# Kernel tuning notes

Measured on AMD Instinct MI355X. Metric: run time of the kernel, lower is better.

Reference implementation:

```python
import jax, jax.numpy as jnp
import numpy as np

B, S, D, H, DO, E, K = 4, 2048, 1024, 4096, 1024, 8, 2


def setup_inputs() -> dict:
    key = jax.random.key(0)
    ks = jax.random.split(key, 5)
    sD = 1.0 / np.sqrt(D)
    sH = 1.0 / np.sqrt(H)
    return {
        "x": jax.random.normal(ks[0], (B, S, D), jnp.float32),
        "gate_w": jax.random.normal(ks[1], (D, E), jnp.float32) * sD,
        "gate_b": jnp.zeros((E,), jnp.float32),
        "w1": jax.random.normal(ks[2], (E, D, H), jnp.float32) * sD,
        "b1": jnp.zeros((E, H), jnp.float32),
        "w2": jax.random.normal(ks[3], (E, H, DO), jnp.float32) * sH,
        "b2": jnp.zeros((E, DO), jnp.float32),
    }


def reference(x, gate_w, gate_b, w1, b1, w2, b2):
    # Eval mode: no gating noise, dropout is identity.
    T = B * S
    xf = x.reshape(T, D)
    logits = xf @ gate_w + gate_b                      # [T, E]
    top_v, top_i = jax.lax.top_k(logits, K)            # [T, K]
    top_w = jax.nn.softmax(top_v, axis=-1)             # softmax over top-k scores
    # scatter top-k weights into dense [T, E] gate weights (indices are distinct)
    weights = jnp.zeros_like(logits).at[jnp.arange(T)[:, None], top_i].set(top_w)
    # dense per-expert MLP, combined with (mostly zero) gate weights —
    # same math as the masked gather/scatter loop in the torch source
    h = jax.nn.relu(jnp.einsum('td,edh->teh', xf, w1) + b1)   # [T, E, H]
    eo = jnp.einsum('teh,eho->teo', h, w2) + b2               # [T, E, DO]
    out = jnp.einsum('te,teo->to', weights, eo).reshape(B, S, DO)
    expert_usage = jnp.bincount(top_i.reshape(-1), length=E)
    return out, weights, expert_usage, top_i
```

## Files before the change

kernel.cpp:

```cpp
#include <hip/hip_runtime.h>
#include <cstdint>
#include <cstddef>

typedef unsigned short u16;
typedef unsigned int u32;
typedef short s16x8 __attribute__((ext_vector_type(8)));
typedef float f32x4 __attribute__((ext_vector_type(4)));

#define T_TOK 8192
#define D_IN  1024
#define H_DIM 4096
#define DO_DIM 1024

__device__ __forceinline__ u16 f2bf(float f) {
    u32 u = __float_as_uint(f);
    return (u16)((u + 0x7FFFu + ((u >> 16) & 1u)) >> 16);
}

__device__ __forceinline__ f32x4 mfma16(s16x8 a, s16x8 b, f32x4 c) {
    return __builtin_amdgcn_mfma_f32_16x16x32_bf16(a, b, c, 0, 0, 0);
}

__device__ __forceinline__ void gload16(const void* g, void* l) {
    __builtin_amdgcn_global_load_lds(
        (const __attribute__((address_space(1))) void*)g,
        (__attribute__((address_space(3))) void*)l,
        16, 0, 0);
}

__global__ __launch_bounds__(256) void gate_transpose_kernel(
    const float* __restrict__ x, const float* __restrict__ gw,
    const float* __restrict__ gb, float* __restrict__ weights_out,
    float* __restrict__ topi_out, int* __restrict__ gcounts,
    int* __restrict__ tok_list, int* __restrict__ slot_of_tok,
    const float* __restrict__ w1, const float* __restrict__ w2,
    u16* __restrict__ w1t, u16* __restrict__ w2t,
    int chunk, int HC, int gate_blocks)
{
    __shared__ u16 tile[64][68];
    __shared__ int lcount[8];
    __shared__ int gbase[8];
    __shared__ short tinfo[16][4];

    const int bid = blockIdx.x;
    if (bid < gate_blocks) {
        const int wid = threadIdx.x >> 6;
        const int lane = threadIdx.x & 63;
        const int tbase = bid << 4;
        if (threadIdx.x < 8) lcount[threadIdx.x] = 0;
        __syncthreads();
        for (int j = 0; j < 4; ++j) {
            const int t = tbase + (wid << 2) + j;
            const float* xr = x + ((size_t)t << 10);
            float p[8];
#pragma unroll
            for (int e = 0; e < 8; ++e) p[e] = 0.f;
#pragma unroll
            for (int i = 0; i < 16; ++i) {
                int d = lane + i * 64;
                float xv = xr[d];
                const f32x4 g0 = *(const f32x4*)(gw + d * 8);
                const f32x4 g1 = *(const f32x4*)(gw + d * 8 + 4);
                p[0] += xv * g0[0]; p[1] += xv * g0[1]; p[2] += xv * g0[2]; p[3] += xv * g0[3];
                p[4] += xv * g1[0]; p[5] += xv * g1[1]; p[6] += xv * g1[2]; p[7] += xv * g1[3];
            }
#pragma unroll
            for (int off = 32; off >= 1; off >>= 1) {
#pragma unroll
                for (int e = 0; e < 8; ++e) p[e] += __shfl_xor(p[e], off, 64);
            }
            if (lane == 0) {
                float lg[8];
#pragma unroll
                for (int e = 0; e < 8; ++e) lg[e] = p[e] + gb[e];
                int i0 = 0;
                for (int e = 1; e < 8; ++e) if (lg[e] > lg[i0]) i0 = e;
                int i1 = (i0 == 0) ? 1 : 0;
                for (int e = 0; e < 8; ++e) if (e != i0 && lg[e] > lg[i1]) i1 = e;
                float ex = expf(lg[i1] - lg[i0]);
                float p0 = 1.f / (1.f + ex);
                float p1 = ex / (1.f + ex);
#pragma unroll
                for (int e = 0; e < 8; ++e)
                    weights_out[t * 8 + e] = (e == i0) ? p0 : ((e == i1) ? p1 : 0.f);
                topi_out[t * 2 + 0] = (float)i0;
                topi_out[t * 2 + 1] = (float)i1;
                int idx = (wid << 2) + j;
                int r0 = atomicAdd(&lcount[i0], 1);
                int r1 = atomicAdd(&lcount[i1], 1);
                tinfo[idx][0] = (short)i0; tinfo[idx][1] = (short)r0;
                tinfo[idx][2] = (short)i1; tinfo[idx][3] = (short)r1;
            }
        }
        __syncthreads();
        if (threadIdx.x < 8)
            gbase[threadIdx.x] = atomicAdd(&gcounts[threadIdx.x * 32], lcount[threadIdx.x]);
        __syncthreads();
        if (threadIdx.x < 16) {
            int t = tbase + threadIdx.x;
            int i0 = tinfo[threadIdx.x][0], r0 = tinfo[threadIdx.x][1];
            int i1 = tinfo[threadIdx.x][2], r1 = tinfo[threadIdx.x][3];
            int pos0 = gbase[i0] + r0;
            int pos1 = gbase[i1] + r1;
            tok_list[(i0 << 13) + pos0] = t;
            slot_of_tok[t * 2 + 0] = (i0 << 13) | pos0;
            tok_list[(i1 << 13) + pos1] = t;
            slot_of_tok[t * 2 + 1] = (i1 << 13) | pos1;
        }
        return;
    }

    const int tid = threadIdx.x;
    const int tiles_h = HC >> 6;
    const int per_e = 32 * tiles_h;
    const int ntile1 = 16 * tiles_h;
    const int b2 = bid - gate_blocks;
    const int e = b2 / per_e;
    const int b = b2 - e * per_e;
    const float* src; u16* dst;
    size_t sstride, dstride;
    int r0, c0;
    if (b < ntile1) {
        int tr = b / tiles_h, tc = b % tiles_h;
        r0 = tr * 64; c0 = tc * 64;
        src = w1 + (size_t)e * D_IN * H_DIM + (size_t)chunk * HC;
        sstride = H_DIM;
        dst = w1t + (size_t)e * HC * D_IN;
        dstride = D_IN;
    } else {
        int tb = b - ntile1;
        int tr = tb / 16, tc = tb % 16;
        r0 = tr * 64; c0 = tc * 64;
        src = w2 + ((size_t)e * H_DIM + (size_t)chunk * HC) * DO_DIM;
        sstride = DO_DIM;
        dst = w2t + (size_t)e * DO_DIM * HC;
        dstride = HC;
    }
#pragma unroll
    for (int i = 0; i < 4; ++i) {
        int flat = i * 1024 + tid * 4;
        int rr = flat >> 6, cc = flat & 63;
        float4 v = *(const float4*)(src + (size_t)(r0 + rr) * sstride + c0 + cc);
        ushort4 h4;
        h4.x = f2bf(v.x); h4.y = f2bf(v.y); h4.z = f2bf(v.z); h4.w = f2bf(v.w);
        *(ushort4*)&tile[rr][cc] = h4;
    }
    __syncthreads();
#pragma unroll
    for (int i = 0; i < 4; ++i) {
        int flat = i * 1024 + tid * 4;
        int rr = flat >> 6, cc = flat & 63;
        ushort4 o;
        o.x = tile[cc + 0][rr]; o.y = tile[cc + 1][rr];
        o.z = tile[cc + 2][rr]; o.w = tile[cc + 3][rr];
        *(ushort4*)(dst + (size_t)(c0 + rr) * dstride + r0 + cc) = o;
    }
}

__global__ void zero_counts_kernel(int* c) { c[threadIdx.x] = 0; }

__global__ void scan_kernel(const int* __restrict__ gcounts, int* __restrict__ counts,
                            int* __restrict__ base, float* __restrict__ usage_out,
                            int* __restrict__ rbt) {
    if (threadIdx.x == 0) {
        int acc = 0;
        for (int e = 0; e < 8; ++e) {
            int c = gcounts[e * 32];
            counts[e] = c;
            base[e] = acc;
            acc += c;
            usage_out[e] = (float)c;
        }
        int nrb = 0;
        for (int e = 0; e < 8; ++e) {
            int nb = (counts[e] + 127) >> 7;
            for (int rb = 0; rb < nb; ++rb) rbt[1 + nrb++] = (e << 16) | rb;
        }
        rbt[0] = nrb;
    }
}

__global__ __launch_bounds__(256) void gather_kernel(
    const float* __restrict__ x, const int* __restrict__ slot_of_tok,
    const int* __restrict__ base, u16* __restrict__ xg)
{
    const int t = blockIdx.x;
    const int s = slot_of_tok[t * 2 + blockIdx.y];
    const int slot = base[s >> 13] + (s & 8191);
    const int d = threadIdx.x * 4;
    float4 v = *(const float4*)(x + ((size_t)t << 10) + d);
    ushort4 h;
    h.x = f2bf(v.x); h.y = f2bf(v.y); h.z = f2bf(v.z); h.w = f2bf(v.w);
    *(ushort4*)(xg + ((size_t)slot << 10) + d) = h;
}


__device__ __forceinline__ void stage6s(const char* const gA[2], const char* const gB[4],
                                        char* slab, int koff, int tid) {
    char* l = slab + __builtin_amdgcn_readfirstlane((tid >> 6) << 10);
#pragma unroll
    for (int i = 0; i < 2; ++i) gload16(gA[i] + koff, l + i * 8192);
#pragma unroll
    for (int i = 0; i < 4; ++i) gload16(gB[i] + koff, l + 16384 + i * 8192);
}

#define MFMA_BLOCK(S) do { \
    s16x8 la0[4], lb0[4], la1[4], lb1[4]; \
    _Pragma("unroll") \
    for (int m = 0; m < 4; ++m) la0[m] = *(const s16x8*)((S) + aoff0 + m * 2048); \
    _Pragma("unroll") \
    for (int n = 0; n < 4; ++n) lb0[n] = *(const s16x8*)((S) + boff0 + n * 2048); \
    _Pragma("unroll") \
    for (int m = 0; m < 4; ++m) la1[m] = *(const s16x8*)((S) + aoff1 + m * 2048); \
    _Pragma("unroll") \
    for (int n = 0; n < 4; ++n) lb1[n] = *(const s16x8*)((S) + boff1 + n * 2048); \
    __builtin_amdgcn_s_setprio(1); \
    _Pragma("unroll") \
    for (int m = 0; m < 4; ++m) \
        _Pragma("unroll") \
        for (int n = 0; n < 4; ++n) acc[m][n] = mfma16(la0[m], lb0[n], acc[m][n]); \
    _Pragma("unroll") \
    for (int m = 0; m < 4; ++m) \
        _Pragma("unroll") \
        for (int n = 0; n < 4; ++n) acc[m][n] = mfma16(la1[m], lb1[n], acc[m][n]); \
    __builtin_amdgcn_s_setprio(0); } while(0)

#define GEMM_CORE(NTV) \
    const int arow = (wm << 6) + (lane & 15); \
    const int brow = (wn << 6) + (lane & 15); \
    const int ko = (lane >> 4) << 4; \
    const int aoff0 = arow * 128 + (ko ^ ((arow & 7) << 4)); \
    const int aoff1 = arow * 128 + ((64 + ko) ^ ((arow & 7) << 4)); \
    const int boff0 = 16384 + brow * 128 + (ko ^ ((brow & 7) << 4)); \
    const int boff1 = 16384 + brow * 128 + ((64 + ko) ^ ((brow & 7) << 4)); \
    f32x4 acc[4][4]; \
    _Pragma("unroll") \
    for (int m = 0; m < 4; ++m) \
        _Pragma("unroll") \
        for (int n = 0; n < 4; ++n) acc[m][n] = f32x4{0.f, 0.f, 0.f, 0.f}; \
    stage6s(gA, gB, sm, 0, tid); \
    stage6s(gA, gB, sm + 49152, 128, tid); \
    int cs = 0; \
    _Pragma("unroll 1") \
    for (int t = 0; t < (NTV); ++t) { \
        if (t + 1 < (NTV)) asm volatile("s_waitcnt vmcnt(6)" ::: "memory"); \
        else               asm volatile("s_waitcnt vmcnt(0)" ::: "memory"); \
        __builtin_amdgcn_sched_barrier(0); \
        __builtin_amdgcn_s_barrier(); \
        __builtin_amdgcn_sched_barrier(0); \
        if (t + 2 < (NTV)) { \
            int ss = cs + 2; if (ss >= 3) ss -= 3; \
            stage6s(gA, gB, sm + ss * 49152, (t + 2) * 128, tid); \
        } \
        const char* S_ = sm + cs * 49152; \
        MFMA_BLOCK(S_); \
        cs = cs + 1; if (cs == 3) cs = 0; \
    }

__global__ __launch_bounds__(512) void gemm1_kernel(
    const u16* __restrict__ xg, const u16* __restrict__ w1t,
    const float* __restrict__ b1, u16* __restrict__ hbuf,
    const int* __restrict__ counts, const int* __restrict__ base,
    const int* __restrict__ rbt, int chunk, int HC)
{
    const int nrb = rbt[0];
    if (blockIdx.y >= nrb) return;
    const int ent = rbt[1 + blockIdx.y];
    const int e = ent >> 16;
    const int row0 = (ent & 0xffff) << 7;
    const int n_e = counts[e];
    const int sbase = base[e];
    const int col0 = blockIdx.x << 8;
    const int tid = threadIdx.x;
    const int lane = tid & 63;
    const int wv = tid >> 6;
    const int wm = wv >> 2;
    const int wn = wv & 3;

    __shared__ char sm[147456];

    const int scb_ = ((tid & 7) << 4) ^ (((tid >> 3) & 7) << 4);
    const char* gA[2]; const char* gB[4];
#pragma unroll
    for (int i = 0; i < 2; ++i) {
        int slot = sbase + row0 + i * 64 + (tid >> 3);
        slot = slot < 16383 ? slot : 16383;
        gA[i] = (const char*)xg + ((size_t)slot << 11) + scb_;
    }
#pragma unroll
    for (int i = 0; i < 4; ++i) {
        int hrow = col0 + i * 64 + (tid >> 3);
        gB[i] = (const char*)w1t + (((size_t)e * HC + hrow) << 11) + scb_;
    }

    GEMM_CORE(16)

    const int crow = (wm << 6) + ((lane >> 4) << 2);
    const int ccol = (wn << 6) + (lane & 15);
    float bias_n[4];
#pragma unroll
    for (int n = 0; n < 4; ++n)
        bias_n[n] = b1[(e << 12) + chunk * HC + col0 + ccol + n * 16];
#pragma unroll
    for (int m = 0; m < 4; ++m) {
#pragma unroll
        for (int j = 0; j < 4; ++j) {
            int r = row0 + crow + m * 16 + j;
            if (r < n_e) {
                u16* dst = hbuf + (size_t)(sbase + r) * HC + col0;
#pragma unroll
                for (int n = 0; n < 4; ++n) {
                    float v = acc[m][n][j] + bias_n[n];
                    v = v > 0.f ? v : 0.f;
                    dst[ccol + n * 16] = f2bf(v);
                }
            }
        }
    }
}

__global__ __launch_bounds__(512) void gemm2_kernel(
    const u16* __restrict__ hbuf, const u16* __restrict__ w2t,
    const float* __restrict__ b2, float* __restrict__ eo,
    const int* __restrict__ counts, const int* __restrict__ base,
    const int* __restrict__ rbt, int chunk, int HC)
{
    const int nrb = rbt[0];
    if (blockIdx.y >= nrb) return;
    const int ent = rbt[1 + blockIdx.y];
    const int e = ent >> 16;
    const int row0 = (ent & 0xffff) << 7;
    const int n_e = counts[e];
    const int sbase = base[e];
    const int col0 = blockIdx.x << 8;
    const int tid = threadIdx.x;
    const int lane = tid & 63;
    const int wv = tid >> 6;
    const int wm = wv >> 2;
    const int wn = wv & 3;

    __shared__ char sm[147456];

    const int scb_ = ((tid & 7) << 4) ^ (((tid >> 3) & 7) << 4);
    const char* gA[2]; const char* gB[4];
#pragma unroll
    for (int i = 0; i < 2; ++i) {
        int slot = sbase + row0 + i * 64 + (tid >> 3);
        slot = slot < 16383 ? slot : 16383;
        gA[i] = (const char*)hbuf + (((size_t)slot * HC) << 1) + scb_;
    }
#pragma unroll
    for (int i = 0; i < 4; ++i) {
        int orow = col0 + i * 64 + (tid >> 3);
        gB[i] = (const char*)w2t + ((((size_t)(e << 10) + orow) * HC) << 1) + scb_;
    }

    const int NT = HC >> 6;
    GEMM_CORE(NT)

    const int crow = (wm << 6) + ((lane >> 4) << 2);
    const int ccol = (wn << 6) + (lane & 15);
    float bias_n[4];
#pragma unroll
    for (int n = 0; n < 4; ++n)
        bias_n[n] = (chunk == 0) ? b2[(e << 10) + col0 + ccol + n * 16] : 0.f;
#pragma unroll
    for (int m = 0; m < 4; ++m) {
#pragma unroll
        for (int j = 0; j < 4; ++j) {
            int r = row0 + crow + m * 16 + j;
            if (r < n_e) {
                float* dst = eo + ((size_t)(sbase + r) << 10) + col0;
#pragma unroll
                for (int n = 0; n < 4; ++n) {
                    int c = ccol + n * 16;
                    float v = acc[m][n][j] + bias_n[n];
                    if (chunk) v += dst[c];
                    dst[c] = v;
                }
            }
        }
    }
}

__global__ __launch_bounds__(256) void combine_kernel(
    const float* __restrict__ eo, const float* __restrict__ weights,
    const int* __restrict__ slot_of_tok, const int* __restrict__ base,
    float* __restrict__ out)
{
    const int t = blockIdx.x;
    const int tid = threadIdx.x;
    int s0 = slot_of_tok[t * 2], s1 = slot_of_tok[t * 2 + 1];
    int e0 = s0 >> 13, e1 = s1 >> 13;
    int c0 = base[e0] + (s0 & 8191);
    int c1 = base[e1] + (s1 & 8191);
    float w0 = weights[t * 8 + e0];
    float w1 = weights[t * 8 + e1];
    int c = tid * 4;
    f32x4 a = *(const f32x4*)(eo + ((size_t)c0 << 10) + c);
    f32x4 b = *(const f32x4*)(eo + ((size_t)c1 << 10) + c);
    f32x4 r;
    r[0] = w0 * a[0] + w1 * b[0];
    r[1] = w0 * a[1] + w1 * b[1];
    r[2] = w0 * a[2] + w1 * b[2];
    r[3] = w0 * a[3] + w1 * b[3];
    *(f32x4*)(out + ((size_t)t << 10) + c) = r;
}

extern "C" void kernel_launch(void* const* d_in, const int* in_sizes, int n_in,
                              void* d_out, int out_size, void* d_ws, size_t ws_size,
                              hipStream_t stream)
{
    const float* x      = (const float*)d_in[0];
    const float* gate_w = (const float*)d_in[1];
    const float* gate_b = (const float*)d_in[2];
    const float* w1     = (const float*)d_in[3];
    const float* b1     = (const float*)d_in[4];
    const float* w2     = (const float*)d_in[5];
    const float* b2     = (const float*)d_in[6];

    float* out         = (float*)d_out;
    float* weights_out = out + (size_t)T_TOK * DO_DIM;
    float* usage_out   = weights_out + (size_t)T_TOK * 8;
    float* topi_out    = usage_out + 8;

    char* p = (char*)d_ws;
    int* gcounts = (int*)p;      p += 1024;
    int* counts = (int*)p;       p += 256;
    int* base   = (int*)p;       p += 256;
    int* rbt    = (int*)p;       p += 1024;
    int* tok_list = (int*)p;     p += (size_t)8 * 8192 * 4;
    int* slot_of_tok = (int*)p;  p += (size_t)8192 * 2 * 4;
    const size_t fixed = (size_t)(p - (char*)d_ws);

    const size_t xg_bytes = (size_t)16384 * 1024 * 2;
    const size_t eo_bytes = (size_t)16384 * 1024 * 4;
    int HC;
    if      (ws_size >= fixed + xg_bytes + eo_bytes + (size_t)65536 * 4096) HC = 4096;
    else if (ws_size >= fixed + xg_bytes + eo_bytes + (size_t)65536 * 2048) HC = 2048;
    else if (ws_size >= fixed + xg_bytes + eo_bytes + (size_t)65536 * 1024) HC = 1024;
    else                                                                    HC = 512;

    u16* xg   = (u16*)p; p += xg_bytes;
    u16* w1t  = (u16*)p; p += (size_t)8 * HC * 1024 * 2;
    u16* w2t  = (u16*)p; p += (size_t)8 * 1024 * HC * 2;
    u16* hbuf = (u16*)p; p += (size_t)16384 * HC * 2;
    float* eo = (float*)p;

    const int tiles_h = HC / 64;
    const int per_e = 32 * tiles_h;
    const int trans_blocks = 8 * per_e;

    zero_counts_kernel<<<1, 256, 0, stream>>>(gcounts);
    gate_transpose_kernel<<<512 + trans_blocks, 256, 0, stream>>>(
        x, gate_w, gate_b, weights_out, topi_out, gcounts, tok_list, slot_of_tok,
        w1, w2, w1t, w2t, 0, HC, 512);
    scan_kernel<<<1, 64, 0, stream>>>(gcounts, counts, base, usage_out, rbt);
    gather_kernel<<<dim3(T_TOK, 2), 256, 0, stream>>>(x, slot_of_tok, base, xg);

    const int NC = H_DIM / HC;
    for (int c = 0; c < NC; ++c) {
        if (c > 0)
            gate_transpose_kernel<<<trans_blocks, 256, 0, stream>>>(
                x, gate_w, gate_b, weights_out, topi_out, gcounts, tok_list, slot_of_tok,
                w1, w2, w1t, w2t, c, HC, 0);
        gemm1_kernel<<<dim3(HC / 256, 136, 1), 512, 0, stream>>>(xg, w1t, b1, hbuf,
                                                                 counts, base, rbt, c, HC);
        gemm2_kernel<<<dim3(DO_DIM / 256, 136, 1), 512, 0, stream>>>(hbuf, w2t, b2, eo,
                                                                     counts, base, rbt, c, HC);
    }
    combine_kernel<<<T_TOK, 256, 0, stream>>>(eo, weights_out, slot_of_tok, base, out);
}
```

Baseline: 513.8 us.

## Split hidden dim in halves and co-schedule gemm1 tail with gemm2 first half

When the whole hidden dimension fits in one chunk, the expert MLP is split into two halves along H. A combined kernel runs the second half of the first GEMM alongside the second GEMM's partial reduction over the first half, and a final launch accumulates the second half. The aim is to reduce wave-quantization tails and idle CUs between dependent GEMM launches. It adds an extra read-modify-write of the fp32 expert output and an extra launch, and relies on cross-launch ordering for correctness.

```diff
diff --git a/kernel.cpp b/kernel.cpp
--- a/kernel.cpp
+++ b/kernel.cpp
@@ -257,28 +257,26 @@
         cs = cs + 1; if (cs == 3) cs = 0; \
     }
 
-__global__ __launch_bounds__(512) void gemm1_kernel(
-    const u16* __restrict__ xg, const u16* __restrict__ w1t,
+__device__ __forceinline__ void run_gemm1(
+    char* sm, const u16* __restrict__ xg, const u16* __restrict__ w1t,
     const float* __restrict__ b1, u16* __restrict__ hbuf,
     const int* __restrict__ counts, const int* __restrict__ base,
-    const int* __restrict__ rbt, int chunk, int HC)
+    const int* __restrict__ rbt, int bx, int by, int hoff, int bo, int HC)
 {
     const int nrb = rbt[0];
-    if (blockIdx.y >= nrb) return;
-    const int ent = rbt[1 + blockIdx.y];
+    if (by >= nrb) return;
+    const int ent = rbt[1 + by];
     const int e = ent >> 16;
     const int row0 = (ent & 0xffff) << 7;
     const int n_e = counts[e];
     const int sbase = base[e];
-    const int col0 = blockIdx.x << 8;
+    const int col0 = hoff + (bx << 8);
     const int tid = threadIdx.x;
     const int lane = tid & 63;
     const int wv = tid >> 6;
     const int wm = wv >> 2;
     const int wn = wv & 3;
 
-    __shared__ char sm[147456];
-
     const int scb_ = ((tid & 7) << 4) ^ (((tid >> 3) & 7) << 4);
     const char* gA[2]; const char* gB[4];
 #pragma unroll
@@ -300,7 +298,7 @@
     float bias_n[4];
 #pragma unroll
     for (int n = 0; n < 4; ++n)
-        bias_n[n] = b1[(e << 12) + chunk * HC + col0 + ccol + n * 16];
+        bias_n[n] = b1[(e << 12) + bo + (bx << 8) + ccol + n * 16];
 #pragma unroll
     for (int m = 0; m < 4; ++m) {
 #pragma unroll
@@ -319,51 +317,48 @@
     }
 }
 
-__global__ __launch_bounds__(512) void gemm2_kernel(
-    const u16* __restrict__ hbuf, const u16* __restrict__ w2t,
+__device__ __forceinline__ void run_gemm2(
+    char* sm, const u16* __restrict__ hbuf, const u16* __restrict__ w2t,
     const float* __restrict__ b2, float* __restrict__ eo,
     const int* __restrict__ counts, const int* __restrict__ base,
-    const int* __restrict__ rbt, int chunk, int HC)
+    const int* __restrict__ rbt, int bx, int by, int kbase, int NTV, int kflag, int HC)
 {
     const int nrb = rbt[0];
-    if (blockIdx.y >= nrb) return;
-    const int ent = rbt[1 + blockIdx.y];
+    if (by >= nrb) return;
+    const int ent = rbt[1 + by];
     const int e = ent >> 16;
     const int row0 = (ent & 0xffff) << 7;
     const int n_e = counts[e];
     const int sbase = base[e];
-    const int col0 = blockIdx.x << 8;
+    const int col0 = bx << 8;
     const int tid = threadIdx.x;
     const int lane = tid & 63;
     const int wv = tid >> 6;
     const int wm = wv >> 2;
     const int wn = wv & 3;
 
-    __shared__ char sm[147456];
-
     const int scb_ = ((tid & 7) << 4) ^ (((tid >> 3) & 7) << 4);
     const char* gA[2]; const char* gB[4];
 #pragma unroll
     for (int i = 0; i < 2; ++i) {
         int slot = sbase + row0 + i * 64 + (tid >> 3);
         slot = slot < 16383 ? slot : 16383;
-        gA[i] = (const char*)hbuf + (((size_t)slot * HC) << 1) + scb_;
+        gA[i] = (const char*)hbuf + (((size_t)slot * HC + kbase) << 1) + scb_;
     }
 #pragma unroll
     for (int i = 0; i < 4; ++i) {
         int orow = col0 + i * 64 + (tid >> 3);
-        gB[i] = (const char*)w2t + ((((size_t)(e << 10) + orow) * HC) << 1) + scb_;
-    }
-
-    const int NT = HC >> 6;
-    GEMM_CORE(NT)
+        gB[i] = (const char*)w2t + ((((size_t)(e << 10) + orow) * HC + kbase) << 1) + scb_;
+    }
+
+    GEMM_CORE(NTV)
 
     const int crow = (wm << 6) + ((lane >> 4) << 2);
     const int ccol = (wn << 6) + (lane & 15);
     float bias_n[4];
 #pragma unroll
     for (int n = 0; n < 4; ++n)
-        bias_n[n] = (chunk == 0) ? b2[(e << 10) + col0 + ccol + n * 16] : 0.f;
+        bias_n[n] = (kflag == 0) ? b2[(e << 10) + col0 + ccol + n * 16] : 0.f;
 #pragma unroll
     for (int m = 0; m < 4; ++m) {
 #pragma unroll
@@ -375,12 +370,51 @@
                 for (int n = 0; n < 4; ++n) {
                     int c = ccol + n * 16;
                     float v = acc[m][n][j] + bias_n[n];
-                    if (chunk) v += dst[c];
+                    if (kflag) v += dst[c];
                     dst[c] = v;
                 }
             }
         }
     }
+}
+
+__global__ __launch_bounds__(512) void gemm1_kernel(
+    const u16* __restrict__ xg, const u16* __restrict__ w1t,
+    const float* __restrict__ b1, u16* __restrict__ hbuf,
+    const int* __restrict__ counts, const int* __restrict__ base,
+    const int* __restrict__ rbt, int hoff, int bo, int HC)
+{
+    __shared__ char sm[147456];
+    run_gemm1(sm, xg, w1t, b1, hbuf, counts, base, rbt,
+              blockIdx.x, blockIdx.y, hoff, bo, HC);
+}
+
+__global__ __launch_bounds__(512) void gemm2_kernel(
+    const u16* __restrict__ hbuf, const u16* __restrict__ w2t,
+    const float* __restrict__ b2, float* __restrict__ eo,
+    const int* __restrict__ counts, const int* __restrict__ base,
+    const int* __restrict__ rbt, int kbase, int NTV, int kflag, int HC)
+{
+    __shared__ char sm[147456];
+    run_gemm2(sm, hbuf, w2t, b2, eo, counts, base, rbt,
+              blockIdx.x, blockIdx.y, kbase, NTV, kflag, HC);
+}
+
+__global__ __launch_bounds__(512) void gemm_mid_kernel(
+    const u16* __restrict__ xg, const u16* __restrict__ w1t,
+    const float* __restrict__ b1, u16* __restrict__ hbuf,
+    const u16* __restrict__ w2t, const float* __restrict__ b2,
+    float* __restrict__ eo, const int* __restrict__ counts,
+    const int* __restrict__ base, const int* __restrict__ rbt,
+    int g1x, int hoff, int kNTV, int HC)
+{
+    __shared__ char sm[147456];
+    if ((int)blockIdx.x < g1x)
+        run_gemm1(sm, xg, w1t, b1, hbuf, counts, base, rbt,
+                  blockIdx.x, blockIdx.y, hoff, hoff, HC);
+    else
+        run_gemm2(sm, hbuf, w2t, b2, eo, counts, base, rbt,
+                  blockIdx.x - g1x, blockIdx.y, 0, kNTV, 0, HC);
 }
 
 __global__ __launch_bounds__(256) void combine_kernel(
@@ -458,16 +492,27 @@
     scan_kernel<<<1, 64, 0, stream>>>(gcounts, counts, base, usage_out, rbt);
     gather_kernel<<<dim3(T_TOK, 2), 256, 0, stream>>>(x, slot_of_tok, base, xg);
 
-    const int NC = H_DIM / HC;
-    for (int c = 0; c < NC; ++c) {
-        if (c > 0)
-            gate_transpose_kernel<<<trans_blocks, 256, 0, stream>>>(
-                x, gate_w, gate_b, weights_out, topi_out, gcounts, tok_list, slot_of_tok,
-                w1, w2, w1t, w2t, c, HC, 0);
-        gemm1_kernel<<<dim3(HC / 256, 136, 1), 512, 0, stream>>>(xg, w1t, b1, hbuf,
-                                                                 counts, base, rbt, c, HC);
-        gemm2_kernel<<<dim3(DO_DIM / 256, 136, 1), 512, 0, stream>>>(hbuf, w2t, b2, eo,
-                                                                     counts, base, rbt, c, HC);
+    if (HC == 4096) {
+        gemm1_kernel<<<dim3(8, 136), 512, 0, stream>>>(xg, w1t, b1, hbuf,
+                                                       counts, base, rbt, 0, 0, HC);
+        gemm_mid_kernel<<<dim3(12, 136), 512, 0, stream>>>(xg, w1t, b1, hbuf, w2t, b2, eo,
+                                                           counts, base, rbt, 8, 2048, 32, HC);
+        gemm2_kernel<<<dim3(4, 136), 512, 0, stream>>>(hbuf, w2t, b2, eo,
+                                                       counts, base, rbt, 2048, 32, 1, HC);
+    } else {
+        const int NC = H_DIM / HC;
+        for (int c = 0; c < NC; ++c) {
+            if (c > 0)
+                gate_transpose_kernel<<<trans_blocks, 256, 0, stream>>>(
+                    x, gate_w, gate_b, weights_out, topi_out, gcounts, tok_list, slot_of_tok,
+                    w1, w2, w1t, w2t, c, HC, 0);
+            gemm1_kernel<<<dim3(HC / 256, 136, 1), 512, 0, stream>>>(xg, w1t, b1, hbuf,
+                                                                     counts, base, rbt,
+                                                                     0, c * HC, HC);
+            gemm2_kernel<<<dim3(4, 136, 1), 512, 0, stream>>>(hbuf, w2t, b2, eo,
+                                                              counts, base, rbt,
+                                                              0, HC / 64, c > 0 ? 1 : 0, HC);
+        }
     }
     combine_kernel<<<T_TOK, 256, 0, stream>>>(eo, weights_out, slot_of_tok, base, out);
 }
```

After: 580.9 us. 1.13x slower.

## Shrink GEMM tiles to 128x128 with 4 waves and double buffering

Applied to the files above, without the earlier changes.

Both expert GEMM kernels move from a 128x256 tile with 8 waves and a 3-stage LDS ring of 144KB to a 128x128 tile with 4 waves and a 2-stage ring of 64KB. The loop now waits for all loads (vmcnt(0)) before each step instead of keeping one stage in flight. The smaller LDS footprint allows more blocks per CU and the grid doubles along N, which should improve occupancy and load balance across experts. In exchange, operand reuse per tile drops and prefetch depth is shallower, so memory latency is hidden less.

```diff
diff --git a/kernel.cpp b/kernel.cpp
--- a/kernel.cpp
+++ b/kernel.cpp
@@ -195,13 +195,14 @@
 }
 
 
-__device__ __forceinline__ void stage6s(const char* const gA[2], const char* const gB[4],
-                                        char* slab, int koff, int tid) {
+__device__ __forceinline__ void stage4(const char* const gA[4], const char* const gB[4],
+                                       char* slab, int koff, int tid) {
     char* l = slab + __builtin_amdgcn_readfirstlane((tid >> 6) << 10);
 #pragma unroll
-    for (int i = 0; i < 2; ++i) gload16(gA[i] + koff, l + i * 8192);
-#pragma unroll
-    for (int i = 0; i < 4; ++i) gload16(gB[i] + koff, l + 16384 + i * 8192);
+    for (int i = 0; i < 4; ++i) {
+        gload16(gA[i] + koff, l + i * 4096);
+        gload16(gB[i] + koff, l + 16384 + i * 4096);
+    }
 }
 
 #define MFMA_BLOCK(S) do { \
@@ -225,7 +226,7 @@
         for (int n = 0; n < 4; ++n) acc[m][n] = mfma16(la1[m], lb1[n], acc[m][n]); \
     __builtin_amdgcn_s_setprio(0); } while(0)
 
-#define GEMM_CORE(NTV) \
+#define GEMM_CORE2(NTV) \
     const int arow = (wm << 6) + (lane & 15); \
     const int brow = (wn << 6) + (lane & 15); \
     const int ko = (lane >> 4) << 4; \
@@ -238,62 +239,52 @@
     for (int m = 0; m < 4; ++m) \
         _Pragma("unroll") \
         for (int n = 0; n < 4; ++n) acc[m][n] = f32x4{0.f, 0.f, 0.f, 0.f}; \
-    stage6s(gA, gB, sm, 0, tid); \
-    stage6s(gA, gB, sm + 49152, 128, tid); \
-    int cs = 0; \
+    stage4(gA, gB, sm, 0, tid); \
     _Pragma("unroll 1") \
     for (int t = 0; t < (NTV); ++t) { \
-        if (t + 1 < (NTV)) asm volatile("s_waitcnt vmcnt(6)" ::: "memory"); \
-        else               asm volatile("s_waitcnt vmcnt(0)" ::: "memory"); \
+        asm volatile("s_waitcnt vmcnt(0)" ::: "memory"); \
         __builtin_amdgcn_sched_barrier(0); \
         __builtin_amdgcn_s_barrier(); \
         __builtin_amdgcn_sched_barrier(0); \
-        if (t + 2 < (NTV)) { \
-            int ss = cs + 2; if (ss >= 3) ss -= 3; \
-            stage6s(gA, gB, sm + ss * 49152, (t + 2) * 128, tid); \
-        } \
-        const char* S_ = sm + cs * 49152; \
+        if (t + 1 < (NTV)) stage4(gA, gB, sm + ((t + 1) & 1) * 32768, (t + 1) * 128, tid); \
+        const char* S_ = sm + (t & 1) * 32768; \
         MFMA_BLOCK(S_); \
-        cs = cs + 1; if (cs == 3) cs = 0; \
-    }
-
-__global__ __launch_bounds__(512) void gemm1_kernel(
+    }
+
+__global__ __launch_bounds__(256) void gemm1_kernel(
     const u16* __restrict__ xg, const u16* __restrict__ w1t,
     const float* __restrict__ b1, u16* __restrict__ hbuf,
     const int* __restrict__ counts, const int* __restrict__ base,
     const int* __restrict__ rbt, int chunk, int HC)
 {
     const int nrb = rbt[0];
-    if (blockIdx.y >= nrb) return;
+    if ((int)blockIdx.y >= nrb) return;
     const int ent = rbt[1 + blockIdx.y];
     const int e = ent >> 16;
     const int row0 = (ent & 0xffff) << 7;
     const int n_e = counts[e];
     const int sbase = base[e];
-    const int col0 = blockIdx.x << 8;
+    const int col0 = blockIdx.x << 7;
     const int tid = threadIdx.x;
     const int lane = tid & 63;
     const int wv = tid >> 6;
-    const int wm = wv >> 2;
-    const int wn = wv & 3;
-
-    __shared__ char sm[147456];
+    const int wm = wv >> 1;
+    const int wn = wv & 1;
+
+    __shared__ char sm[65536];
 
     const int scb_ = ((tid & 7) << 4) ^ (((tid >> 3) & 7) << 4);
-    const char* gA[2]; const char* gB[4];
-#pragma unroll
-    for (int i = 0; i < 2; ++i) {
-        int slot = sbase + row0 + i * 64 + (tid >> 3);
+    const char* gA[4]; const char* gB[4];
+#pragma unroll
+    for (int i = 0; i < 4; ++i) {
+        int slot = sbase + row0 + i * 32 + (tid >> 3);
         slot = slot < 16383 ? slot : 16383;
         gA[i] = (const char*)xg + ((size_t)slot << 11) + scb_;
-    }
-#pragma unroll
-    for (int i = 0; i < 4; ++i) {
-        int hrow = col0 + i * 64 + (tid >> 3);
+        int hrow = col0 + i * 32 + (tid >> 3);
         gB[i] = (const char*)w1t + (((size_t)e * HC + hrow) << 11) + scb_;
     }
 
-    GEMM_CORE(16)
+    GEMM_CORE2(16)
 
     const int crow = (wm << 6) + ((lane >> 4) << 2);
     const int ccol = (wn << 6) + (lane & 15);
@@ -319,44 +310,41 @@
     }
 }
 
-__global__ __launch_bounds__(512) void gemm2_kernel(
+__global__ __launch_bounds__(256) void gemm2_kernel(
     const u16* __restrict__ hbuf, const u16* __restrict__ w2t,
     const float* __restrict__ b2, float* __restrict__ eo,
     const int* __restrict__ counts, const int* __restrict__ base,
     const int* __restrict__ rbt, int chunk, int HC)
 {
     const int nrb = rbt[0];
-    if (blockIdx.y >= nrb) return;
+    if ((int)blockIdx.y >= nrb) return;
     const int ent = rbt[1 + blockIdx.y];
     const int e = ent >> 16;
     const int row0 = (ent & 0xffff) << 7;
     const int n_e = counts[e];
     const int sbase = base[e];
-    const int col0 = blockIdx.x << 8;
+    const int col0 = blockIdx.x << 7;
     const int tid = threadIdx.x;
     const int lane = tid & 63;
     const int wv = tid >> 6;
-    const int wm = wv >> 2;
-    const int wn = wv & 3;
-
-    __shared__ char sm[147456];
+    const int wm = wv >> 1;
+    const int wn = wv & 1;
+
+    __shared__ char sm[65536];
 
     const int scb_ = ((tid & 7) << 4) ^ (((tid >> 3) & 7) << 4);
-    const char* gA[2]; const char* gB[4];
-#pragma unroll
-    for (int i = 0; i < 2; ++i) {
-        int slot = sbase + row0 + i * 64 + (tid >> 3);
+    const char* gA[4]; const char* gB[4];
+#pragma unroll
+    for (int i = 0; i < 4; ++i) {
+        int slot = sbase + row0 + i * 32 + (tid >> 3);
         slot = slot < 16383 ? slot : 16383;
         gA[i] = (const char*)hbuf + (((size_t)slot * HC) << 1) + scb_;
-    }
-#pragma unroll
-    for (int i = 0; i < 4; ++i) {
-        int orow = col0 + i * 64 + (tid >> 3);
+        int orow = col0 + i * 32 + (tid >> 3);
         gB[i] = (const char*)w2t + ((((size_t)(e << 10) + orow) * HC) << 1) + scb_;
     }
 
     const int NT = HC >> 6;
-    GEMM_CORE(NT)
+    GEMM_CORE2(NT)
 
     const int crow = (wm << 6) + ((lane >> 4) << 2);
     const int ccol = (wn << 6) + (lane & 15);
@@ -464,9 +452,9 @@
             gate_transpose_kernel<<<trans_blocks, 256, 0, stream>>>(
                 x, gate_w, gate_b, weights_out, topi_out, gcounts, tok_list, slot_of_tok,
                 w1, w2, w1t, w2t, c, HC, 0);
-        gemm1_kernel<<<dim3(HC / 256, 136, 1), 512, 0, stream>>>(xg, w1t, b1, hbuf,
+        gemm1_kernel<<<dim3(HC / 128, 136, 1), 256, 0, stream>>>(xg, w1t, b1, hbuf,
                                                                  counts, base, rbt, c, HC);
-        gemm2_kernel<<<dim3(DO_DIM / 256, 136, 1), 512, 0, stream>>>(hbuf, w2t, b2, eo,
+        gemm2_kernel<<<dim3(DO_DIM / 128, 136, 1), 256, 0, stream>>>(hbuf, w2t, b2, eo,
                                                                      counts, base, rbt, c, HC);
     }
     combine_kernel<<<T_TOK, 256, 0, stream>>>(eo, weights_out, slot_of_tok, base, out);
```

After: 546.4 us. 1.06x slower.
